# Performance work log

Hardware: AMD Instinct MI355X
Metric: run time of the kernel (lower is better)

## Reference

```python
import jax, jax.numpy as jnp
import numpy as np
from jax import lax
from jax.scipy.special import erf

EPS = 1e-5
B = 256

def _conv(x, w, stride):
    return lax.conv_general_dilated(x, w, (stride, stride), ((1, 1), (1, 1)),
                                    dimension_numbers=('NCHW', 'OIHW', 'NCHW'))

def lr_conv(x, alpha, betta, bias, stride):
    # Ternary weight distribution (LR-nets): p0 = P(w=0), p1 = P(w=1)
    p0 = jax.nn.sigmoid(alpha)
    p1 = (1.0 - p0) * jax.nn.sigmoid(betta)
    w_mean = 2.0 * p1 + p0 - 1.0          # E[w] = p1 - p_{-1}
    w_var = (1.0 - p0) - w_mean * w_mean  # Var[w] = E[w^2] - E[w]^2
    m = _conv(x, w_mean, stride) + bias[None, :, None, None]
    v = _conv(x * x, w_var, stride)
    return m, v

def sign_prob(m, v):
    # expected sign under CLT Gaussian: 2*Phi(m/sqrt(v)) - 1 = erf(m / sqrt(2 v))
    return erf(m / jnp.sqrt(2.0 * (v + EPS)))

def setup_inputs() -> dict:
    key = jax.random.key(0)
    ks = jax.random.split(key, 32)
    def n(k, shape, s=1.0):
        return jax.random.normal(k, shape, dtype=jnp.float32) * s
    inp = {}
    inp['x'] = n(ks[0], (B, 3, 32, 32))
    shapes = [(128, 3), (128, 128), (256, 128), (256, 256), (512, 256), (512, 512)]
    i = 1
    for li, (co, ci) in enumerate(shapes, start=1):
        inp['a%d' % li] = n(ks[i], (co, ci, 3, 3)); i += 1
        inp['b%d' % li] = n(ks[i], (co, ci, 3, 3)); i += 1
        inp['c%d' % li] = jnp.zeros((co,), jnp.float32)
    inp['bn_gamma'] = jnp.ones((512,), jnp.float32)
    inp['bn_beta'] = jnp.zeros((512,), jnp.float32)
    inp['fc1_w'] = n(ks[20], (1024, 8192), 0.01)
    inp['fc1_b'] = jnp.zeros((1024,), jnp.float32)
    inp['fc2_w'] = n(ks[21], (10, 1024), 0.03)
    inp['fc2_b'] = jnp.zeros((10,), jnp.float32)
    inp['noise6'] = n(ks[22], (B, 512, 4, 4))
    return inp

def reference(x, a1, b1, c1, a2, b2, c2, a3, b3, c3, a4, b4, c4, a5, b5, c5,
              a6, b6, c6, bn_gamma, bn_beta, fc1_w, fc1_b, fc2_w, fc2_b, noise6):
    h = x
    for (a, bt, c, s) in [(a1, b1, c1, 1), (a2, b2, c2, 2), (a3, b3, c3, 1),
                          (a4, b4, c4, 2), (a5, b5, c5, 1)]:
        m, v = lr_conv(h, a, bt, c, s)
        h = sign_prob(m, v)
    m, v = lr_conv(h, a6, b6, c6, 2)          # output_sample=True layer
    z = m + jnp.sqrt(v + EPS) * noise6        # reparameterized Gaussian sample
    mu = jnp.mean(z, axis=(0, 2, 3), keepdims=True)
    var = jnp.var(z, axis=(0, 2, 3), keepdims=True)
    z = bn_gamma[None, :, None, None] * (z - mu) / jnp.sqrt(var + EPS) + bn_beta[None, :, None, None]
    z = jax.nn.relu(z).reshape(z.shape[0], -1)  # [B, 8192]
    z = jax.nn.relu(z @ fc1_w.T + fc1_b)
    return z @ fc2_w.T + fc2_b
```

## Files before the change

kernel.cpp:

```cpp
#include <hip/hip_runtime.h>
#include <hip/hip_bf16.h>
#include <math.h>

#define EPS 1e-5f

typedef __hip_bfloat16 bf16;
typedef short s16x8 __attribute__((ext_vector_type(8)));
typedef float f32x4 __attribute__((ext_vector_type(4)));

constexpr int ilog2c(int v) { return v <= 1 ? 0 : 1 + ilog2c(v >> 1); }

__device__ __forceinline__ float ldin(const void* p, size_t i, int isbf) {
    return isbf ? __bfloat162float(((const bf16*)p)[i]) : ((const float*)p)[i];
}
__device__ __forceinline__ float b2f_bits(short s) {
    unsigned u = ((unsigned)(unsigned short)s) << 16;
    return __builtin_bit_cast(float, u);
}
__device__ __forceinline__ uint4 sqpk4(uint4 u) {
    uint4 r;
    unsigned* up = (unsigned*)&u;
    unsigned* rp = (unsigned*)&r;
#pragma unroll
    for (int k = 0; k < 4; k++) {
        unsigned w = up[k];
        float lo = __builtin_bit_cast(float, w << 16);
        float hi = __builtin_bit_cast(float, w & 0xffff0000u);
        lo *= lo; hi *= hi;
        unsigned ul = __builtin_bit_cast(unsigned, lo) + 0x8000u;
        unsigned uh = __builtin_bit_cast(unsigned, hi) + 0x8000u;
        rp[k] = (ul >> 16) | (uh & 0xffff0000u);
    }
    return r;
}

__device__ __forceinline__ void dma16(const void* g, void* l) {
    __builtin_amdgcn_global_load_lds(
        (const __attribute__((address_space(1))) void*)g,
        (__attribute__((address_space(3))) void*)l, 16, 0, 0);
}

__global__ __launch_bounds__(64) void detect_kernel(const void* __restrict__ x,
                                                    int* __restrict__ flags,
                                                    char* __restrict__ gA,
                                                    char* __restrict__ gB) {
    const unsigned* w = (const unsigned*)x;
    unsigned word = w[threadIdx.x];
    int e = (word >> 23) & 0xFF;
    bool ok = (word == 0u) || (e >= 0x70 && e <= 0x8E);
    unsigned long long m = __ballot(ok);
    if (threadIdx.x == 0) flags[0] = (__popcll(m) >= 32) ? 0 : 1;
    if (threadIdx.x < 16) ((uint4*)gA)[threadIdx.x] = (uint4){0, 0, 0, 0};
    else if (threadIdx.x < 32) ((uint4*)gB)[threadIdx.x - 16] = (uint4){0, 0, 0, 0};
}

__global__ __launch_bounds__(256) void prep_w_l1(
    const void* __restrict__ alpha, const void* __restrict__ betta,
    const int* __restrict__ flags, float* __restrict__ wmv, int n)
{
    int i = blockIdx.x * 256 + threadIdx.x;
    if (i >= n) return;
    int fl = flags[0];
    float a = ldin(alpha, i, fl), b = ldin(betta, i, fl);
    float p0 = 1.f / (1.f + expf(-a));
    float p1 = (1.f - p0) / (1.f + expf(-b));
    float m = 2.f * p1 + p0 - 1.f;
    wmv[i] = m;
    wmv[n + i] = (1.f - p0) - m * m;
}

__global__ __launch_bounds__(256) void prep_w_r(
    const void* __restrict__ alpha, const void* __restrict__ betta,
    const int* __restrict__ flags, bf16* __restrict__ wmr, bf16* __restrict__ wvr,
    int lc, int n)
{
    int o = blockIdx.x * 256 + threadIdx.x;
    if (o >= n) return;
    int fl = flags[0];
    int cotap = o >> lc;
    int ci = o & ((1 << lc) - 1);
    int co = cotap / 9;
    int tap = cotap - co * 9;
    int i = (((co << lc) + ci) * 9) + tap;
    float a = ldin(alpha, i, fl), b = ldin(betta, i, fl);
    float p0 = 1.f / (1.f + expf(-a));
    float p1 = (1.f - p0) / (1.f + expf(-b));
    float m = 2.f * p1 + p0 - 1.f;
    float v = (1.f - p0) - m * m;
    wmr[o] = __float2bfloat16(m);
    wvr[o] = __float2bfloat16(v);
}

__global__ __launch_bounds__(256) void permute_fc1(
    const void* __restrict__ w, const int* __restrict__ flags, bf16* __restrict__ wp)
{
    __shared__ float L[8192];
    const int fl = flags[0];
    int tid = threadIdx.x;
    int o = blockIdx.x;
    size_t srow = (size_t)o * 8192;
    for (int c = tid; c < 512; c += 256) {
        float v[16];
        if (fl) {
            const uint4* s = (const uint4*)((const bf16*)w + srow + c * 16);
            uint4 u0 = s[0], u1 = s[1];
            const unsigned short* h0 = (const unsigned short*)&u0;
            const unsigned short* h1 = (const unsigned short*)&u1;
#pragma unroll
            for (int j = 0; j < 8; j++) { v[j] = b2f_bits((short)h0[j]); v[8 + j] = b2f_bits((short)h1[j]); }
        } else {
            const float4* s = (const float4*)((const float*)w + srow + c * 16);
#pragma unroll
            for (int j = 0; j < 4; j++) {
                float4 t4 = s[j];
                v[j * 4 + 0] = t4.x; v[j * 4 + 1] = t4.y; v[j * 4 + 2] = t4.z; v[j * 4 + 3] = t4.w;
            }
        }
#pragma unroll
        for (int hw = 0; hw < 16; hw++) L[hw * 512 + c] = v[hw];
    }
    __syncthreads();
    for (int j = 0; j < 32; j++) {
        int idx = j * 256 + tid;
        wp[srow + idx] = __float2bfloat16(L[idx]);
    }
}

__global__ __launch_bounds__(256) void l1_conv(
    const void* __restrict__ x, const float* __restrict__ wmv,
    const void* __restrict__ bias, const int* __restrict__ flags,
    bf16* __restrict__ out)
{
    __shared__ float Xs[64][28];
    const int fl = flags[0];
    int tid = threadIdx.x;
    int pos0 = blockIdx.x * 64;
    int b = pos0 >> 10;
    for (int u = tid; u < 576; u += 256) {
        int p = u / 9, r = u - p * 9;
        int ci = r / 3, kh = r - ci * 3;
        int pos = pos0 + p;
        int oh = (pos >> 5) & 31, ow = pos & 31;
        int ih = oh - 1 + kh;
        bool okh = (unsigned)ih < 32u;
        size_t base = ((size_t)(b * 3 + ci) * 32 + ih) * 32;
#pragma unroll
        for (int kw = 0; kw < 3; kw++) {
            int iw = ow - 1 + kw;
            float v = (okh && (unsigned)iw < 32u) ? ldin(x, base + iw, fl) : 0.f;
            Xs[p][ci * 9 + kh * 3 + kw] = v;
        }
    }
    int c = tid & 127, pg = tid >> 7;
    float wm[27], wv[27];
#pragma unroll
    for (int k = 0; k < 27; k++) {
        wm[k] = wmv[c * 27 + k];
        wv[k] = wmv[3456 + c * 27 + k];
    }
    float bs = ldin(bias, c, fl);
    __syncthreads();
    for (int it = 0; it < 32; it++) {
        int p = it * 2 + pg;
        float aM = 0.f, aV = 0.f;
#pragma unroll
        for (int k = 0; k < 27; k++) {
            float xv = Xs[p][k];
            aM = fmaf(xv, wm[k], aM);
            aV = fmaf(xv * xv, wv[k], aV);
        }
        out[(size_t)(pos0 + p) * 128 + c] =
            __float2bfloat16(erff((aM + bs) * rsqrtf(2.f * (aV + EPS))));
    }
}

template<int CI, int CO, int H, int W, int S, int OH, int OW, int ACT, int COT>
__global__ __launch_bounds__(256, 2) void conv_gemm(
    const char* __restrict__ xreg,
    int zpoff,
    const bf16* __restrict__ wmr,
    const bf16* __restrict__ wvr,
    const void* __restrict__ bias, const void* __restrict__ noise,
    const int* __restrict__ flags, void* __restrict__ outp)
{
    constexpr int OHW = OH * OW;
    constexpr int KC = CI / 32;
    constexpr int NC = 9 * KC;
    constexpr int WJ = COT / 32;
    constexpr int NW = COT / 16;
    constexpr int XB = 128 * 64;
    constexpr int WB = COT * 64;
    constexpr int BUFB = XB + 2 * WB;
    constexpr int LOHW = ilog2c(OHW), LOW = ilog2c(OW);
    static_assert(NC % 3 == 0, "");

    __shared__ __align__(16) char smem[3 * BUFB];

    const int tid = threadIdx.x;
    const int lane = tid & 63, wv_ = tid >> 6;
    const int q = lane >> 4, l15 = lane & 15;
    const int pw = (wv_ >> 1) * 64, cw = (wv_ & 1) * (16 * WJ);
    const int c0 = blockIdx.y * COT;
    const int bx128 = blockIdx.x * 128;

    const int sl   = (lane & 7) ^ (lane >> 3);
    const int row2 = 2 * (lane >> 3) + (sl >> 2);
    const int u16b = (sl & 3) * 16;

    int xb[4], ohS[4], owS[4];
#pragma unroll
    for (int kk = 0; kk < 4; kk++) {
        int P = bx128 + 16 * ((wv_ & 1) * 4 + kk) + row2;
        int bi = P >> LOHW;
        ohS[kk] = ((P >> LOW) & (OH - 1)) * S - 1;
        owS[kk] = (P & (OW - 1)) * S - 1;
        xb[kk] = bi * (H * W * CI * 2);
    }
    const char* wsb = (const char*)((wv_ == 3) ? wvr : wmr)
                      + (size_t)(c0 + row2) * (9 * CI * 2) + u16b;
    const int wdoff = XB + ((wv_ == 3) ? WB : 0);

    const int lA = (l15 >> 1) * 128 + (((((l15 & 1) << 2) | q) ^ (l15 >> 1)) << 4);
    const int abase = pw * 64 + lA;
    const int bbase = cw * 64 + lA;

    f32x4 accM[4][WJ], accV[4][WJ];
#pragma unroll
    for (int i = 0; i < 4; i++)
#pragma unroll
        for (int j = 0; j < WJ; j++) {
            accM[i][j] = (f32x4){0.f, 0.f, 0.f, 0.f};
            accV[i][j] = (f32x4){0.f, 0.f, 0.f, 0.f};
        }

    auto stage = [&](int t, int nb) {
        char* buf = smem + nb * BUFB;
        if (wv_ < 2) {
            const int tap = t / KC, kci = (t - tap * KC) * 64;
            const int kh = tap / 3, kw2 = tap - 3 * kh;
#pragma unroll
            for (int kk = 0; kk < 4; kk++) {
                int ih = ohS[kk] + kh, iw = owS[kk] + kw2;
                bool ok = ((unsigned)ih < (unsigned)H) && ((unsigned)iw < (unsigned)W);
                int off = xb[kk] + (ih * W + iw) * (CI * 2) + kci + u16b;
                off = ok ? off : zpoff;
                dma16(xreg + off, buf + ((wv_ & 1) * 4 + kk) * 1024);
            }
        } else {
            const char* s = wsb + t * 64;
            char* d = buf + wdoff;
#pragma unroll
            for (int k = 0; k < NW; k++)
                dma16(s + (size_t)k * (16 * 9 * CI * 2), d + k * 1024);
        }
    };

    auto compute = [&](int nb) {
        const char* buf = smem + nb * BUFB;
        s16x8 a[4], aq[4];
#pragma unroll
        for (int i = 0; i < 4; i++) {
            a[i] = *(const s16x8*)(buf + abase + i * 1024);
            uint4 u = *(const uint4*)&a[i];
            uint4 uq = sqpk4(u);
            aq[i] = *(const s16x8*)&uq;
        }
#pragma unroll
        for (int j = 0; j < WJ; j++) {
            s16x8 bm = *(const s16x8*)(buf + XB + bbase + j * 1024);
            s16x8 bv = *(const s16x8*)(buf + XB + WB + bbase + j * 1024);
#pragma unroll
            for (int i = 0; i < 4; i++) {
                accM[i][j] = __builtin_amdgcn_mfma_f32_16x16x32_bf16(a[i],  bm, accM[i][j], 0, 0, 0);
                accV[i][j] = __builtin_amdgcn_mfma_f32_16x16x32_bf16(aq[i], bv, accV[i][j], 0, 0, 0);
            }
        }
    };

    auto step = [&](int t, int nb, int nb2) {
        if (t == NC - 1)
            asm volatile("s_waitcnt vmcnt(0) lgkmcnt(0)\n\ts_barrier" ::: "memory");
        else if (COT == 128 && wv_ >= 2)
            asm volatile("s_waitcnt vmcnt(8) lgkmcnt(0)\n\ts_barrier" ::: "memory");
        else
            asm volatile("s_waitcnt vmcnt(4) lgkmcnt(0)\n\ts_barrier" ::: "memory");
        if (t + 2 < NC) stage(t + 2, nb2);
        compute(nb);
    };

    stage(0, 0);
    stage(1, 1);
    for (int tt = 0; tt < NC; tt += 3) {
        step(tt, 0, 2);
        step(tt + 1, 1, 0);
        step(tt + 2, 2, 1);
    }

    __syncthreads();
    const int fl = flags[0];
    if constexpr (ACT == 0) {
        bf16* Lact = (bf16*)smem;
        constexpr int LCB = ilog2c(COT * 2);
#pragma unroll
        for (int j = 0; j < WJ; j++) {
            int co = c0 + cw + j * 16 + l15;
            float bs = ldin(bias, co, fl);
#pragma unroll
            for (int i = 0; i < 4; i++) {
#pragma unroll
                for (int r = 0; r < 4; r++) {
                    int PPl = pw + i * 16 + q * 4 + r;
                    float mm = accM[i][j][r] + bs, vv = accV[i][j][r];
                    Lact[PPl * COT + cw + j * 16 + l15] =
                        __float2bfloat16(erff(mm * rsqrtf(2.f * (vv + EPS))));
                }
            }
        }
        __syncthreads();
        constexpr int NST = (128 * COT * 2) / 4096;
#pragma unroll
        for (int k = 0; k < NST; k++) {
            int f = k * 4096 + tid * 16;
            int rowl = f >> LCB;
            int colb = f & ((COT * 2) - 1);
            uint4 va = *(const uint4*)((char*)smem + f);
            size_t gb = ((size_t)(bx128 + rowl) * CO + c0) * 2 + colb;
            *(uint4*)((char*)outp + gb) = va;
        }
    } else {
#pragma unroll
        for (int j = 0; j < WJ; j++) {
            int co = c0 + cw + j * 16 + l15;
            float bs = ldin(bias, co, fl);
#pragma unroll
            for (int i = 0; i < 4; i++) {
#pragma unroll
                for (int r = 0; r < 4; r++) {
                    int PP = bx128 + pw + i * 16 + q * 4 + r;
                    float mm = accM[i][j][r] + bs, vv = accV[i][j][r];
                    int bb = PP / OHW, hw = PP % OHW;
                    float nz = ldin(noise, ((size_t)bb * CO + co) * OHW + hw, fl);
                    ((float*)outp)[(size_t)PP * CO + co] = mm + sqrtf(vv + EPS) * nz;
                }
            }
        }
    }
}

__global__ __launch_bounds__(256) void fc1_gemm_sk(
    const bf16* __restrict__ A, const bf16* __restrict__ Wp,
    float* __restrict__ part)
{
    __shared__ bf16 Xs[128 * 40];
    __shared__ bf16 Ws[128 * 40];
    int tid = threadIdx.x;
    int lane = tid & 63, wv_ = tid >> 6;
    int q = lane >> 4, l15 = lane & 15;
    const int pw = (wv_ >> 1) * 64, cw = (wv_ & 1) * 64;
    const int p0 = blockIdx.x * 128, c0 = blockIdx.y * 128;
    const int kb = blockIdx.z * 1024;
    const int row_i = tid >> 1, half = tid & 1;

    f32x4 acc[4][4];
#pragma unroll
    for (int i = 0; i < 4; i++)
#pragma unroll
        for (int j = 0; j < 4; j++) acc[i][j] = (f32x4){0.f, 0.f, 0.f, 0.f};

    for (int k0 = kb; k0 < kb + 1024; k0 += 32) {
        __syncthreads();
        {
            const uint4* s = (const uint4*)(A + (size_t)(p0 + row_i) * 8192 + k0 + half * 16);
            uint4* d = (uint4*)(Xs + row_i * 40 + half * 16);
            d[0] = s[0]; d[1] = s[1];
        }
        {
            const uint4* s = (const uint4*)(Wp + (size_t)(c0 + row_i) * 8192 + k0 + half * 16);
            uint4* d = (uint4*)(Ws + row_i * 40 + half * 16);
            d[0] = s[0]; d[1] = s[1];
        }
        __syncthreads();
        s16x8 a[4], bb[4];
#pragma unroll
        for (int i = 0; i < 4; i++) {
            a[i]  = *(const s16x8*)(Xs + (pw + i * 16 + l15) * 40 + q * 8);
            bb[i] = *(const s16x8*)(Ws + (cw + i * 16 + l15) * 40 + q * 8);
        }
#pragma unroll
        for (int i = 0; i < 4; i++)
#pragma unroll
            for (int j = 0; j < 4; j++)
                acc[i][j] = __builtin_amdgcn_mfma_f32_16x16x32_bf16(a[i], bb[j], acc[i][j], 0, 0, 0);
    }

    float* pbase = part + (size_t)blockIdx.z * 256 * 1024;
#pragma unroll
    for (int j = 0; j < 4; j++) {
        int co = c0 + cw + j * 16 + l15;
#pragma unroll
        for (int i = 0; i < 4; i++) {
            f32x4 m4 = acc[i][j];
#pragma unroll
            for (int r = 0; r < 4; r++) {
                int P = p0 + pw + i * 16 + q * 4 + r;
                pbase[(size_t)P * 1024 + co] = m4[r];
            }
        }
    }
}

__global__ __launch_bounds__(256) void fc1_reduce(
    const float* __restrict__ part, const void* __restrict__ bias,
    const int* __restrict__ flags, float* __restrict__ out)
{
    int i = blockIdx.x * 256 + threadIdx.x;
    float s = 0.f;
#pragma unroll
    for (int k = 0; k < 8; k++) s += part[(size_t)k * 262144 + i];
    out[i] = fmaxf(s + ldin(bias, i & 1023, flags[0]), 0.f);
}

__global__ __launch_bounds__(256) void bn_part(const float* __restrict__ z,
                                               float4* __restrict__ partial)
{
    int blk = blockIdx.x;
    int t = threadIdx.x;
    float s0 = 0, ss0 = 0, s1 = 0, ss1 = 0;
    for (int p = 0; p < 32; p++) {
        float2 v = ((const float2*)z)[((size_t)(blk * 32 + p)) * 256 + t];
        s0 += v.x; ss0 += v.x * v.x;
        s1 += v.y; ss1 += v.y * v.y;
    }
    partial[blk * 256 + t] = make_float4(s0, ss0, s1, ss1);
}

__global__ __launch_bounds__(512) void bn_fin(
    const float4* __restrict__ partial, const void* __restrict__ gamma,
    const void* __restrict__ beta, const int* __restrict__ flags,
    float* __restrict__ sc, float* __restrict__ sh)
{
    int c = threadIdx.x;
    float s = 0, ss = 0;
    for (int j = 0; j < 128; j++) {
        float4 pv = partial[j * 256 + (c >> 1)];
        s += (c & 1) ? pv.z : pv.x;
        ss += (c & 1) ? pv.w : pv.y;
    }
    float mean = s * (1.f / 4096.f);
    float var = ss * (1.f / 4096.f) - mean * mean;
    int fl = flags[0];
    float scale = ldin(gamma, c, fl) * rsqrtf(var + EPS);
    sc[c] = scale;
    sh[c] = ldin(beta, c, fl) - mean * scale;
}

__global__ __launch_bounds__(256) void bn_apply(
    const float* __restrict__ z, const float* __restrict__ sc,
    const float* __restrict__ sh, bf16* __restrict__ zr)
{
    int i = blockIdx.x * 256 + threadIdx.x;
    int c = i & 511;
    float v = z[i] * sc[c] + sh[c];
    zr[i] = __float2bfloat16(fmaxf(v, 0.f));
}

__global__ __launch_bounds__(640) void fc2_kernel(
    const float* __restrict__ A, const void* __restrict__ W,
    const void* __restrict__ bias, const int* __restrict__ flags,
    void* __restrict__ out)
{
    const int fl = flags[0];
    int n = blockIdx.x;
    int o = threadIdx.x >> 6;
    int lane = threadIdx.x & 63;
    const float* a = A + (size_t)n * 1024;
    size_t wbase = (size_t)o * 1024;
    float s = 0.f;
    for (int i = lane; i < 1024; i += 64) s = fmaf(a[i], ldin(W, wbase + i, fl), s);
#pragma unroll
    for (int off = 32; off > 0; off >>= 1) s += __shfl_down(s, off);
    if (lane == 0) {
        float v = s + ldin(bias, o, fl);
        if (fl) ((bf16*)out)[n * 10 + o] = __float2bfloat16(v);
        else    ((float*)out)[n * 10 + o] = v;
    }
}

extern "C" void kernel_launch(void* const* d_in, const int* in_sizes, int n_in,
                              void* d_out, int out_size, void* d_ws, size_t ws_size,
                              hipStream_t stream)
{
    const void* x = d_in[0];
    const void *al[6], *be[6], *bi[6];
    for (int l = 0; l < 6; l++) {
        al[l] = d_in[1 + 3 * l];
        be[l] = d_in[2 + 3 * l];
        bi[l] = d_in[3 + 3 * l];
    }
    const void* bn_gamma = d_in[19];
    const void* bn_beta  = d_in[20];
    const void* fc1_w = d_in[21];
    const void* fc1_b = d_in[22];
    const void* fc2_w = d_in[23];
    const void* fc2_b = d_in[24];
    const void* noise = d_in[25];

    char* base = (char*)d_ws;
    size_t off = 0;
    auto alloc = [&](size_t bytes) { void* p = base + off; off += (bytes + 255) & ~(size_t)255; return p; };
    int* flags = (int*)alloc(256);
    float* w1 = (float*)alloc(2 * 3456 * sizeof(float));
    const int SwLC[5] = {7, 7, 8, 8, 9};
    const size_t Sw[5] = {147456, 294912, 589824, 1179648, 2359296};
    bf16 *wmr[5], *wvr[5];
    for (int l = 0; l < 5; l++) {
        wmr[l] = (bf16*)alloc(Sw[l] * sizeof(bf16));
        wvr[l] = (bf16*)alloc(Sw[l] * sizeof(bf16));
    }
    bf16* Wp   = (bf16*)alloc((size_t)1024 * 8192 * sizeof(bf16));
    float4* part = (float4*)alloc((size_t)128 * 256 * sizeof(float4));
    float* bnsc = (float*)alloc(512 * sizeof(float));
    float* bnsh = (float*)alloc(512 * sizeof(float));
    float* fc1o = (float*)alloc((size_t)256 * 1024 * sizeof(float));
    bf16* zr   = (bf16*)alloc((size_t)256 * 8192 * sizeof(bf16));

    const int ZPA = 67108864;
    const int ZPB = 16777216;
    char* RA = (char*)alloc((size_t)ZPA + 256);
    char* RB = (char*)alloc((size_t)ZPB + 256);
    float* z = (float*)RB;
    float* fc1part = (float*)(RB + 8388608);

    detect_kernel<<<1, 64, 0, stream>>>(x, flags, RA + ZPA, RB + ZPB);

    prep_w_l1<<<14, 256, 0, stream>>>(al[0], be[0], flags, w1, 3456);
    for (int l = 0; l < 5; l++) {
        int n = (int)Sw[l];
        prep_w_r<<<(n + 255) / 256, 256, 0, stream>>>(
            al[l + 1], be[l + 1], flags, wmr[l], wvr[l], SwLC[l], n);
    }
    permute_fc1<<<1024, 256, 0, stream>>>(fc1_w, flags, Wp);

    l1_conv<<<4096, 256, 0, stream>>>(x, w1, bi[0], flags, (bf16*)RA);

    conv_gemm<128, 128, 32, 32, 2, 16, 16, 0, 128><<<dim3(512, 1), 256, 0, stream>>>(
        RA, ZPA, wmr[0], wvr[0], bi[1], nullptr, flags, RB);
    conv_gemm<128, 256, 16, 16, 1, 16, 16, 0, 128><<<dim3(512, 2), 256, 0, stream>>>(
        RB, ZPB, wmr[1], wvr[1], bi[2], nullptr, flags, RA);
    conv_gemm<256, 256, 16, 16, 2, 8, 8, 0, 64><<<dim3(128, 4), 256, 0, stream>>>(
        RA, ZPA, wmr[2], wvr[2], bi[3], nullptr, flags, RB);
    conv_gemm<256, 512, 8, 8, 1, 8, 8, 0, 128><<<dim3(128, 4), 256, 0, stream>>>(
        RB, ZPB, wmr[3], wvr[3], bi[4], nullptr, flags, RA);
    conv_gemm<512, 512, 8, 8, 2, 4, 4, 1, 64><<<dim3(32, 8), 256, 0, stream>>>(
        RA, ZPA, wmr[4], wvr[4], bi[5], noise, flags, z);

    bn_part<<<128, 256, 0, stream>>>(z, part);
    bn_fin<<<1, 512, 0, stream>>>(part, bn_gamma, bn_beta, flags, bnsc, bnsh);
    bn_apply<<<8192, 256, 0, stream>>>(z, bnsc, bnsh, zr);

    fc1_gemm_sk<<<dim3(2, 8, 8), 256, 0, stream>>>(zr, Wp, fc1part);
    fc1_reduce<<<1024, 256, 0, stream>>>(fc1part, fc1_b, flags, fc1o);
    fc2_kernel<<<256, 640, 0, stream>>>(fc1o, fc2_w, fc2_b, flags, d_out);
}
```

Baseline: 738.0 us.

## Shrink conv GEMM tiles to 64 channels and double-buffer for higher occupancy

All conv GEMM layers now use a 64-channel output tile, which doubles the grid in the layers that previously used 128. The LDS pipeline goes from triple to double buffering with a full wait at every barrier, and launch bounds now request 4 blocks per CU. The compute loop is reordered to hold B fragments and square A per row, and the bf16 square-pack uses a perm instruction. The intent is more resident waves to hide latency. The cost is less overlap from the shallower pipeline and more reloading of input tiles across the extra channel blocks.

```diff
diff --git a/kernel.cpp b/kernel.cpp
--- a/kernel.cpp
+++ b/kernel.cpp
@@ -17,20 +17,17 @@
     unsigned u = ((unsigned)(unsigned short)s) << 16;
     return __builtin_bit_cast(float, u);
 }
+__device__ __forceinline__ unsigned sqpk1(unsigned w) {
+    float lo = __builtin_bit_cast(float, w << 16);
+    float hi = __builtin_bit_cast(float, w & 0xffff0000u);
+    lo *= lo; hi *= hi;
+    unsigned ul = __builtin_bit_cast(unsigned, lo) + 0x8000u;
+    unsigned uh = __builtin_bit_cast(unsigned, hi) + 0x8000u;
+    return __builtin_amdgcn_perm(uh, ul, 0x07060302);
+}
 __device__ __forceinline__ uint4 sqpk4(uint4 u) {
     uint4 r;
-    unsigned* up = (unsigned*)&u;
-    unsigned* rp = (unsigned*)&r;
-#pragma unroll
-    for (int k = 0; k < 4; k++) {
-        unsigned w = up[k];
-        float lo = __builtin_bit_cast(float, w << 16);
-        float hi = __builtin_bit_cast(float, w & 0xffff0000u);
-        lo *= lo; hi *= hi;
-        unsigned ul = __builtin_bit_cast(unsigned, lo) + 0x8000u;
-        unsigned uh = __builtin_bit_cast(unsigned, hi) + 0x8000u;
-        rp[k] = (ul >> 16) | (uh & 0xffff0000u);
-    }
+    r.x = sqpk1(u.x); r.y = sqpk1(u.y); r.z = sqpk1(u.z); r.w = sqpk1(u.w);
     return r;
 }
 
@@ -175,7 +172,7 @@
 }
 
 template<int CI, int CO, int H, int W, int S, int OH, int OW, int ACT, int COT>
-__global__ __launch_bounds__(256, 2) void conv_gemm(
+__global__ __launch_bounds__(256, 4) void conv_gemm(
     const char* __restrict__ xreg,
     int zpoff,
     const bf16* __restrict__ wmr,
@@ -192,9 +189,9 @@
     constexpr int WB = COT * 64;
     constexpr int BUFB = XB + 2 * WB;
     constexpr int LOHW = ilog2c(OHW), LOW = ilog2c(OW);
-    static_assert(NC % 3 == 0, "");
-
-    __shared__ __align__(16) char smem[3 * BUFB];
+    static_assert((NC & 1) == 0 && COT == 64, "");
+
+    __shared__ __align__(16) char smem[2 * BUFB];
 
     const int tid = threadIdx.x;
     const int lane = tid & 63, wv_ = tid >> 6;
@@ -257,44 +254,37 @@
 
     auto compute = [&](int nb) {
         const char* buf = smem + nb * BUFB;
-        s16x8 a[4], aq[4];
+        s16x8 bm[WJ], bv[WJ];
+#pragma unroll
+        for (int j = 0; j < WJ; j++) {
+            bm[j] = *(const s16x8*)(buf + XB + bbase + j * 1024);
+            bv[j] = *(const s16x8*)(buf + XB + WB + bbase + j * 1024);
+        }
 #pragma unroll
         for (int i = 0; i < 4; i++) {
-            a[i] = *(const s16x8*)(buf + abase + i * 1024);
-            uint4 u = *(const uint4*)&a[i];
-            uint4 uq = sqpk4(u);
-            aq[i] = *(const s16x8*)&uq;
-        }
-#pragma unroll
-        for (int j = 0; j < WJ; j++) {
-            s16x8 bm = *(const s16x8*)(buf + XB + bbase + j * 1024);
-            s16x8 bv = *(const s16x8*)(buf + XB + WB + bbase + j * 1024);
-#pragma unroll
-            for (int i = 0; i < 4; i++) {
-                accM[i][j] = __builtin_amdgcn_mfma_f32_16x16x32_bf16(a[i],  bm, accM[i][j], 0, 0, 0);
-                accV[i][j] = __builtin_amdgcn_mfma_f32_16x16x32_bf16(aq[i], bv, accV[i][j], 0, 0, 0);
+            s16x8 a = *(const s16x8*)(buf + abase + i * 1024);
+            uint4 uq = sqpk4(*(const uint4*)&a);
+            s16x8 aq = *(const s16x8*)&uq;
+#pragma unroll
+            for (int j = 0; j < WJ; j++) {
+                accM[i][j] = __builtin_amdgcn_mfma_f32_16x16x32_bf16(a,  bm[j], accM[i][j], 0, 0, 0);
+                accV[i][j] = __builtin_amdgcn_mfma_f32_16x16x32_bf16(aq, bv[j], accV[i][j], 0, 0, 0);
             }
         }
     };
 
-    auto step = [&](int t, int nb, int nb2) {
-        if (t == NC - 1)
-            asm volatile("s_waitcnt vmcnt(0) lgkmcnt(0)\n\ts_barrier" ::: "memory");
-        else if (COT == 128 && wv_ >= 2)
-            asm volatile("s_waitcnt vmcnt(8) lgkmcnt(0)\n\ts_barrier" ::: "memory");
-        else
-            asm volatile("s_waitcnt vmcnt(4) lgkmcnt(0)\n\ts_barrier" ::: "memory");
-        if (t + 2 < NC) stage(t + 2, nb2);
-        compute(nb);
-    };
+#define BAR() asm volatile("s_waitcnt vmcnt(0) lgkmcnt(0)\n\ts_barrier" ::: "memory")
 
     stage(0, 0);
-    stage(1, 1);
-    for (int tt = 0; tt < NC; tt += 3) {
-        step(tt, 0, 2);
-        step(tt + 1, 1, 0);
-        step(tt + 2, 2, 1);
-    }
+    for (int t = 0; t < NC; t += 2) {
+        BAR();
+        if (t + 1 < NC) stage(t + 1, 1);
+        compute(0);
+        BAR();
+        if (t + 2 < NC) stage(t + 2, 0);
+        compute(1);
+    }
+#undef BAR
 
     __syncthreads();
     const int fl = flags[0];
@@ -543,13 +533,13 @@
 
     l1_conv<<<4096, 256, 0, stream>>>(x, w1, bi[0], flags, (bf16*)RA);
 
-    conv_gemm<128, 128, 32, 32, 2, 16, 16, 0, 128><<<dim3(512, 1), 256, 0, stream>>>(
+    conv_gemm<128, 128, 32, 32, 2, 16, 16, 0, 64><<<dim3(512, 2), 256, 0, stream>>>(
         RA, ZPA, wmr[0], wvr[0], bi[1], nullptr, flags, RB);
-    conv_gemm<128, 256, 16, 16, 1, 16, 16, 0, 128><<<dim3(512, 2), 256, 0, stream>>>(
+    conv_gemm<128, 256, 16, 16, 1, 16, 16, 0, 64><<<dim3(512, 4), 256, 0, stream>>>(
         RB, ZPB, wmr[1], wvr[1], bi[2], nullptr, flags, RA);
     conv_gemm<256, 256, 16, 16, 2, 8, 8, 0, 64><<<dim3(128, 4), 256, 0, stream>>>(
         RA, ZPA, wmr[2], wvr[2], bi[3], nullptr, flags, RB);
-    conv_gemm<256, 512, 8, 8, 1, 8, 8, 0, 128><<<dim3(128, 4), 256, 0, stream>>>(
+    conv_gemm<256, 512, 8, 8, 1, 8, 8, 0, 64><<<dim3(128, 8), 256, 0, stream>>>(
         RB, ZPB, wmr[3], wvr[3], bi[4], nullptr, flags, RA);
     conv_gemm<512, 512, 8, 8, 2, 4, 4, 1, 64><<<dim3(32, 8), 256, 0, stream>>>(
         RA, ZPA, wmr[4], wvr[4], bi[5], noise, flags, z);
```

New measurement: 764.0 us. 1.04x slower.
